# Performance work log

Hardware: AMD Instinct MI355X
Metric: run time of the kernel (lower is better)

The kernel has to match this reference:

```python
import jax, jax.numpy as jnp
import numpy as np
from jax import lax

R = 1
EPS = 1e-4
K = 2 * R + 1


def _dir_kernels(r):
    k = 2 * r + 1
    ones = np.ones((k, k), np.float32)
    L = ones.copy(); L[:, r + 1:] = 0
    Rk = ones.copy(); Rk[:, :r] = 0
    U = ones.copy(); U[r + 1:, :] = 0
    D = ones.copy(); D[:r, :] = 0
    # NW/NE/SW/SE clone U/D BEFORE normalization (as in the torch code)
    NW = U.copy(); NW[:, r + 1:] = 0
    NE = U.copy(); NE[:, :r] = 0
    SW = D.copy(); SW[:, r + 1:] = 0
    SE = D.copy(); SE[:, :r] = 0
    half = (r + 1) * k          # normalizer for half windows
    quad = (r + 1) ** 2         # normalizer for quadrant windows
    L, Rk, U, D = L / half, Rk / half, U / half, D / half
    NW, NE, SW, SE = NW / quad, NE / quad, SW / quad, SE / quad
    return jnp.asarray(np.stack([L, Rk, U, D, NW, NE, SW, SE])[:, None])  # [8,1,k,k]


_DN = ('NCHW', 'OIHW', 'NCHW')


def _boxfilter(x, r):
    # replication pad + depthwise ones/(k*k) box filter; x: [N,3,H,W]
    k = 2 * r + 1
    xp = jnp.pad(x, ((0, 0), (0, 0), (r, r), (r, r)), mode='edge')
    w = jnp.full((3, 1, k, k), 1.0 / (k * k), dtype=x.dtype)
    return lax.conv_general_dilated(xp, w, (1, 1), 'VALID',
                                    dimension_numbers=_DN, feature_group_count=3)


def setup_inputs() -> dict:
    key = jax.random.key(0)
    k1, k2, k3 = jax.random.split(key, 3)
    lr_x = jax.random.uniform(k1, (1, 3, 2048, 2048), jnp.float32) * 255.0
    lr_y = jax.random.uniform(k2, (1, 3, 2048, 2048), jnp.float32) * 255.0
    hr_x = jax.random.uniform(k3, (1, 3, 4096, 4096), jnp.float32) * 255.0
    return {"lr_x": lr_x, "lr_y": lr_y, "hr_x": hr_x}


def reference(lr_x, lr_y, hr_x):
    # guided-filter coefficients on the low-res pair
    mean_x = _boxfilter(lr_x, R)
    mean_y = _boxfilter(lr_y, R)
    cov_xy = _boxfilter(lr_x * lr_y, R) - mean_x * mean_y
    var_x = _boxfilter(lr_x * lr_x, R) - mean_x * mean_x
    A = cov_xy / (var_x + EPS)            # [1,3,H,W]
    b = mean_y - A * mean_x               # [1,3,H,W]

    # treat channels as batch: [3,1,H,W]; 8 directional kernels at once
    Wd = _dir_kernels(R)                  # [8,1,k,k]
    A_ = A[0][:, None]
    b_ = b[0][:, None]
    im = lr_x[0][:, None]                 # [3,1,H,W]
    pad = [(R, R), (R, R)]
    convA = lax.conv_general_dilated(A_, Wd, (1, 1), pad, dimension_numbers=_DN)
    convb = lax.conv_general_dilated(b_, Wd, (1, 1), pad, dimension_numbers=_DN)
    d = convA * im + convb - im           # [3,8,H,W] directional residuals

    idx = jnp.argmin(jnp.abs(d), axis=1, keepdims=True)   # [3,1,H,W]
    dm = jnp.take_along_axis(d, idx, axis=1)              # best residual
    res = (dm + im).transpose(1, 0, 2, 3)                 # [1,3,H,W]
    # .int() truncation then clamp to [0,255], back to float
    return jnp.clip(jnp.trunc(res), 0.0, 255.0)
```

## Files before the change

### kernel.cpp

```cpp
#include <hip/hip_runtime.h>
#include <math.h>


#define TX 64
#define TY 16
#define SW (TX + 4)
#define SH (TY + 4)
#define AW (TX + 2)
#define AH (TY + 2)
#define NT 256

__global__ __launch_bounds__(NT) void fgf_fused_kernel(
    const float* __restrict__ x, const float* __restrict__ y,
    float* __restrict__ out, int H, int W)
{
    __shared__ float  sx[SH][SW];
    __shared__ float  sy[SH][SW];
    __shared__ double sA[AH][AW];
    __shared__ double sB[AH][AW];

    const int c   = blockIdx.z;
    const int ox0 = blockIdx.x * TX;
    const int oy0 = blockIdx.y * TY;
    const size_t plane = (size_t)H * (size_t)W;
    const float* xc = x + (size_t)c * plane;
    const float* yc = y + (size_t)c * plane;

    const int tid = threadIdx.y * 64 + threadIdx.x;

    for (int i = tid; i < SH * SW; i += NT) {
        int ly = i / SW, lx = i - ly * SW;
        int gy = oy0 - 2 + ly;
        int gx = ox0 - 2 + lx;
        gy = gy < 0 ? 0 : (gy >= H ? H - 1 : gy);
        gx = gx < 0 ? 0 : (gx >= W ? W - 1 : gx);
        size_t gidx = (size_t)gy * W + gx;
        sx[ly][lx] = xc[gidx];
        sy[ly][lx] = yc[gidx];
    }
    __syncthreads();

    const double inv9 = 1.0 / 9.0;
    for (int i = tid; i < AH * AW; i += NT) {
        int ly = i / AW, lx = i - ly * AW;
        int ay = oy0 - 1 + ly;
        int ax = ox0 - 1 + lx;
        double Av = 0.0, Bv = 0.0;
        if (ay >= 0 && ay < H && ax >= 0 && ax < W) {
            double sumx = 0.0, sumy = 0.0, sumxy = 0.0, sumxx = 0.0;
#pragma unroll
            for (int dy = 0; dy < 3; dy++) {
#pragma unroll
                for (int dx = 0; dx < 3; dx++) {
                    double xv = (double)sx[ly + dy][lx + dx];
                    double yv = (double)sy[ly + dy][lx + dx];
                    sumx  += xv;
                    sumy  += yv;
                    sumxy += xv * yv;
                    sumxx += xv * xv;
                }
            }
            double mx  = sumx * inv9;
            double my  = sumy * inv9;
            double cov = sumxy * inv9 - mx * my;
            double var = sumxx * inv9 - mx * mx;
            Av = cov / (var + 1e-4);
            Bv = my - Av * mx;
        }
        sA[ly][lx] = Av;
        sB[ly][lx] = Bv;
    }
    __syncthreads();

    const double i6 = 1.0 / 6.0;
    const int tx = threadIdx.x;
    for (int ry = threadIdx.y; ry < TY; ry += 4) {
        int yg = oy0 + ry;
        int xg = ox0 + tx;
        if (yg >= H || xg >= W) continue;

        double a00 = sA[ry + 0][tx + 0], a01 = sA[ry + 0][tx + 1], a02 = sA[ry + 0][tx + 2];
        double a10 = sA[ry + 1][tx + 0], a11 = sA[ry + 1][tx + 1], a12 = sA[ry + 1][tx + 2];
        double a20 = sA[ry + 2][tx + 0], a21 = sA[ry + 2][tx + 1], a22 = sA[ry + 2][tx + 2];
        double b00 = sB[ry + 0][tx + 0], b01 = sB[ry + 0][tx + 1], b02 = sB[ry + 0][tx + 2];
        double b10 = sB[ry + 1][tx + 0], b11 = sB[ry + 1][tx + 1], b12 = sB[ry + 1][tx + 2];
        double b20 = sB[ry + 2][tx + 0], b21 = sB[ry + 2][tx + 1], b22 = sB[ry + 2][tx + 2];

        double at0 = a00 + a10, at1 = a01 + a11, at2 = a02 + a12;
        double am0 = a10 + a20, am1 = a11 + a21, am2 = a12 + a22;
        double ac0 = at0 + a20, ac1 = at1 + a21, ac2 = at2 + a22;
        double bt0 = b00 + b10, bt1 = b01 + b11, bt2 = b02 + b12;
        double bm0 = b10 + b20, bm1 = b11 + b21, bm2 = b12 + b22;
        double bc0 = bt0 + b20, bc1 = bt1 + b21, bc2 = bt2 + b22;

        double cA[8], cB[8];
        cA[0] = (ac0 + ac1) * i6;        cB[0] = (bc0 + bc1) * i6;
        cA[1] = (ac1 + ac2) * i6;        cB[1] = (bc1 + bc2) * i6;
        cA[2] = (at0 + at1 + at2) * i6;  cB[2] = (bt0 + bt1 + bt2) * i6;
        cA[3] = (am0 + am1 + am2) * i6;  cB[3] = (bm0 + bm1 + bm2) * i6;
        cA[4] = (at0 + at1) * 0.25;      cB[4] = (bt0 + bt1) * 0.25;
        cA[5] = (at1 + at2) * 0.25;      cB[5] = (bt1 + bt2) * 0.25;
        cA[6] = (am0 + am1) * 0.25;      cB[6] = (bm0 + bm1) * 0.25;
        cA[7] = (am1 + am2) * 0.25;      cB[7] = (bm1 + bm2) * 0.25;

        double im = (double)sx[ry + 2][tx + 2];

        double best_ad = 1.0e300;
        double best_d  = 0.0;
#pragma unroll
        for (int k = 0; k < 8; k++) {
            double d  = cA[k] * im + cB[k] - im;
            double ad = fabs(d);
            if (ad < best_ad) { best_ad = ad; best_d = d; }
        }

        double res = trunc(best_d + im);
        res = fmin(fmax(res, 0.0), 255.0);
        out[(size_t)c * plane + (size_t)yg * W + xg] = (float)res;
    }
}

extern "C" void kernel_launch(void* const* d_in, const int* in_sizes, int n_in,
                              void* d_out, int out_size, void* d_ws, size_t ws_size,
                              hipStream_t stream) {
    const float* lr_x = (const float*)d_in[0];
    const float* lr_y = (const float*)d_in[1];
    float* out = (float*)d_out;

    const int plane = in_sizes[0] / 3;
    const int H = (int)(0.5 + sqrt((double)plane));
    const int W = plane / H;

    dim3 block(64, 4, 1);
    dim3 grid((W + TX - 1) / TX, (H + TY - 1) / TY, 3);
    fgf_fused_kernel<<<grid, block, 0, stream>>>(lr_x, lr_y, out, H, W);
}
```

Baseline: 370.1 us.

## Use sliding-window row reuse and rcp-based division for guided filter coefficients

Each thread now processes four consecutive rows and slides a 3-row window of A/B partial sums down the tile, so each step loads one new row from shared memory instead of nine values per coefficient. The coefficient computation is rewritten algebraically with unnormalized sums and FMAs, and the double-precision division is replaced by a hardware reciprocal refined with two Newton steps. The aim is to cut LDS traffic and the expensive FP64 division. The cost is slightly different rounding, which could flip a truncated output at boundary values.

```diff
diff --git a/kernel.cpp b/kernel.cpp
--- a/kernel.cpp
+++ b/kernel.cpp
@@ -10,12 +10,25 @@
 #define AH (TY + 2)
 #define NT 256
 
+__device__ __forceinline__ double fast_rcp(double v) {
+#if __has_builtin(__builtin_amdgcn_rcp)
+    double r = __builtin_amdgcn_rcp(v);
+#else
+    double r = 1.0 / v;
+#endif
+    double e = fma(-v, r, 1.0);
+    r = fma(r, e, r);
+    e = fma(-v, r, 1.0);
+    r = fma(r, e, r);
+    return r;
+}
+
 __global__ __launch_bounds__(NT) void fgf_fused_kernel(
     const float* __restrict__ x, const float* __restrict__ y,
     float* __restrict__ out, int H, int W)
 {
-    __shared__ float  sx[SH][SW];
-    __shared__ float  sy[SH][SW];
+    __shared__ float  sxs[SH][SW];
+    __shared__ float  sys[SH][SW];
     __shared__ double sA[AH][AW];
     __shared__ double sB[AH][AW];
 
@@ -35,88 +48,109 @@
         gy = gy < 0 ? 0 : (gy >= H ? H - 1 : gy);
         gx = gx < 0 ? 0 : (gx >= W ? W - 1 : gx);
         size_t gidx = (size_t)gy * W + gx;
-        sx[ly][lx] = xc[gidx];
-        sy[ly][lx] = yc[gidx];
+        sxs[ly][lx] = xc[gidx];
+        sys[ly][lx] = yc[gidx];
     }
     __syncthreads();
 
-    const double inv9 = 1.0 / 9.0;
+    const double EPS81 = 81.0 * 1.0e-4;
+    const double INV9  = 1.0 / 9.0;
     for (int i = tid; i < AH * AW; i += NT) {
         int ly = i / AW, lx = i - ly * AW;
         int ay = oy0 - 1 + ly;
         int ax = ox0 - 1 + lx;
         double Av = 0.0, Bv = 0.0;
         if (ay >= 0 && ay < H && ax >= 0 && ax < W) {
-            double sumx = 0.0, sumy = 0.0, sumxy = 0.0, sumxx = 0.0;
+            double sx4 = 0.0, sy4 = 0.0, sxy = 0.0, sxx = 0.0;
 #pragma unroll
             for (int dy = 0; dy < 3; dy++) {
 #pragma unroll
                 for (int dx = 0; dx < 3; dx++) {
-                    double xv = (double)sx[ly + dy][lx + dx];
-                    double yv = (double)sy[ly + dy][lx + dx];
-                    sumx  += xv;
-                    sumy  += yv;
-                    sumxy += xv * yv;
-                    sumxx += xv * xv;
+                    double xv = (double)sxs[ly + dy][lx + dx];
+                    double yv = (double)sys[ly + dy][lx + dx];
+                    sx4 += xv;
+                    sy4 += yv;
+                    sxy = fma(xv, yv, sxy);
+                    sxx = fma(xv, xv, sxx);
                 }
             }
-            double mx  = sumx * inv9;
-            double my  = sumy * inv9;
-            double cov = sumxy * inv9 - mx * my;
-            double var = sumxx * inv9 - mx * mx;
-            Av = cov / (var + 1e-4);
-            Bv = my - Av * mx;
+            double num = fma(-sx4, sy4, 9.0 * sxy);
+            double den = fma(-sx4, sx4, fma(9.0, sxx, EPS81));
+            Av = num * fast_rcp(den);
+            Bv = fma(-Av, sx4, sy4) * INV9;
         }
         sA[ly][lx] = Av;
         sB[ly][lx] = Bv;
     }
     __syncthreads();
 
-    const double i6 = 1.0 / 6.0;
+    const double I6 = 1.0 / 6.0;
     const int tx = threadIdx.x;
-    for (int ry = threadIdx.y; ry < TY; ry += 4) {
-        int yg = oy0 + ry;
-        int xg = ox0 + tx;
-        if (yg >= H || xg >= W) continue;
+    const int g  = threadIdx.y;
+    const int r0 = g * 4;
+    const int xg = ox0 + tx;
+    const bool xok = (xg < W);
 
-        double a00 = sA[ry + 0][tx + 0], a01 = sA[ry + 0][tx + 1], a02 = sA[ry + 0][tx + 2];
-        double a10 = sA[ry + 1][tx + 0], a11 = sA[ry + 1][tx + 1], a12 = sA[ry + 1][tx + 2];
-        double a20 = sA[ry + 2][tx + 0], a21 = sA[ry + 2][tx + 1], a22 = sA[ry + 2][tx + 2];
-        double b00 = sB[ry + 0][tx + 0], b01 = sB[ry + 0][tx + 1], b02 = sB[ry + 0][tx + 2];
-        double b10 = sB[ry + 1][tx + 0], b11 = sB[ry + 1][tx + 1], b12 = sB[ry + 1][tx + 2];
-        double b20 = sB[ry + 2][tx + 0], b21 = sB[ry + 2][tx + 1], b22 = sB[ry + 2][tx + 2];
+    double tA[3], mA[3], pA[3], tB[3], mB[3], pB[3];
+#pragma unroll
+    for (int cc = 0; cc < 3; cc++) {
+        double a0 = sA[r0 + 0][tx + cc];
+        double a1 = sA[r0 + 1][tx + cc];
+        double a2 = sA[r0 + 2][tx + cc];
+        tA[cc] = a0 + a1; mA[cc] = a1 + a2; pA[cc] = a2;
+        double b0 = sB[r0 + 0][tx + cc];
+        double b1 = sB[r0 + 1][tx + cc];
+        double b2 = sB[r0 + 2][tx + cc];
+        tB[cc] = b0 + b1; mB[cc] = b1 + b2; pB[cc] = b2;
+    }
 
-        double at0 = a00 + a10, at1 = a01 + a11, at2 = a02 + a12;
-        double am0 = a10 + a20, am1 = a11 + a21, am2 = a12 + a22;
-        double ac0 = at0 + a20, ac1 = at1 + a21, ac2 = at2 + a22;
-        double bt0 = b00 + b10, bt1 = b01 + b11, bt2 = b02 + b12;
-        double bm0 = b10 + b20, bm1 = b11 + b21, bm2 = b12 + b22;
-        double bc0 = bt0 + b20, bc1 = bt1 + b21, bc2 = bt2 + b22;
+#pragma unroll
+    for (int step = 0; step < 4; step++) {
+        const int r  = r0 + step;
+        const int yg = oy0 + r;
+        if (xok && yg < H) {
+            double fA0 = tA[0] + pA[0], fA1 = tA[1] + pA[1], fA2 = tA[2] + pA[2];
+            double fB0 = tB[0] + pB[0], fB1 = tB[1] + pB[1], fB2 = tB[2] + pB[2];
 
-        double cA[8], cB[8];
-        cA[0] = (ac0 + ac1) * i6;        cB[0] = (bc0 + bc1) * i6;
-        cA[1] = (ac1 + ac2) * i6;        cB[1] = (bc1 + bc2) * i6;
-        cA[2] = (at0 + at1 + at2) * i6;  cB[2] = (bt0 + bt1 + bt2) * i6;
-        cA[3] = (am0 + am1 + am2) * i6;  cB[3] = (bm0 + bm1 + bm2) * i6;
-        cA[4] = (at0 + at1) * 0.25;      cB[4] = (bt0 + bt1) * 0.25;
-        cA[5] = (at1 + at2) * 0.25;      cB[5] = (bt1 + bt2) * 0.25;
-        cA[6] = (am0 + am1) * 0.25;      cB[6] = (bm0 + bm1) * 0.25;
-        cA[7] = (am1 + am2) * 0.25;      cB[7] = (bm1 + bm2) * 0.25;
+            double t01A = tA[0] + tA[1], t12A = tA[1] + tA[2];
+            double m01A = mA[0] + mA[1], m12A = mA[1] + mA[2];
+            double t01B = tB[0] + tB[1], t12B = tB[1] + tB[2];
+            double m01B = mB[0] + mB[1], m12B = mB[1] + mB[2];
 
-        double im = (double)sx[ry + 2][tx + 2];
+            double cA[8], cB[8];
+            cA[0] = (fA0 + fA1) * I6;      cB[0] = (fB0 + fB1) * I6;
+            cA[1] = (fA1 + fA2) * I6;      cB[1] = (fB1 + fB2) * I6;
+            cA[2] = (t01A + tA[2]) * I6;   cB[2] = (t01B + tB[2]) * I6;
+            cA[3] = (m01A + mA[2]) * I6;   cB[3] = (m01B + mB[2]) * I6;
+            cA[4] = t01A * 0.25;           cB[4] = t01B * 0.25;
+            cA[5] = t12A * 0.25;           cB[5] = t12B * 0.25;
+            cA[6] = m01A * 0.25;           cB[6] = m01B * 0.25;
+            cA[7] = m12A * 0.25;           cB[7] = m12B * 0.25;
 
-        double best_ad = 1.0e300;
-        double best_d  = 0.0;
+            double im = (double)sxs[r + 2][tx + 2];
+
+            double best_ad = 1.0e300, best_d = 0.0;
 #pragma unroll
-        for (int k = 0; k < 8; k++) {
-            double d  = cA[k] * im + cB[k] - im;
-            double ad = fabs(d);
-            if (ad < best_ad) { best_ad = ad; best_d = d; }
+            for (int k = 0; k < 8; k++) {
+                double d  = fma(cA[k], im, cB[k]) - im;
+                double ad = fabs(d);
+                if (ad < best_ad) { best_ad = ad; best_d = d; }
+            }
+
+            double res = trunc(best_d + im);
+            res = fmin(fmax(res, 0.0), 255.0);
+            out[(size_t)c * plane + (size_t)yg * W + xg] = (float)res;
         }
 
-        double res = trunc(best_d + im);
-        res = fmin(fmax(res, 0.0), 255.0);
-        out[(size_t)c * plane + (size_t)yg * W + xg] = (float)res;
+        if (step < 3) {
+#pragma unroll
+            for (int cc = 0; cc < 3; cc++) {
+                double nA = sA[r0 + step + 3][tx + cc];
+                double nB = sB[r0 + step + 3][tx + cc];
+                tA[cc] = mA[cc]; mA[cc] = pA[cc] + nA; pA[cc] = nA;
+                tB[cc] = mB[cc]; mB[cc] = pB[cc] + nB; pB[cc] = nB;
+            }
+        }
     }
 }
 
```

After: 357.7 us. 3.3% less time.
